# Kernel optimization log

Measured on AMD Instinct MI355X. Metric: run time of the kernel, lower is better.

The kernel has to match this reference:

```python
import jax, jax.numpy as jnp
import numpy as np

INPUT_DIM = 512
OUTPUT_DIM = 128
MAX_DEPTH = 5          # internal nodes at depths 0..4, leaves at depth 5
BATCH = 16384
N_INT = 2**MAX_DEPTH - 1        # 31 internal nodes (heap order: node i children 2i+1, 2i+2)
N_ALL = 2**(MAX_DEPTH + 1) - 1  # 63 nodes total, each owns a leaf vector


def setup_inputs() -> dict:
    key = jax.random.key(0)
    k0, k1, k2, k3, k4 = jax.random.split(key, 5)
    x = jax.random.normal(k0, (BATCH, INPUT_DIM), dtype=jnp.float32)
    lim = 1.0 / np.sqrt(INPUT_DIM)  # torch nn.Linear default init range
    W = jax.random.uniform(k1, (N_INT, 2, INPUT_DIM), jnp.float32, -lim, lim)
    b = jax.random.uniform(k2, (N_INT, 2), jnp.float32, -lim, lim)
    # gamma initialized to [0.5, 0.5] in the module; perturb slightly so it's not degenerate
    gamma = 0.5 + 0.02 * jax.random.normal(k3, (N_INT, 2), dtype=jnp.float32)
    leaf = jax.random.normal(k4, (N_ALL, OUTPUT_DIM), dtype=jnp.float32)
    return {"x": x, "W": W, "b": b, "gamma": gamma, "leaf": leaf}


def reference(x, W, b, gamma, leaf):
    """Level-by-level (bottom-up) vectorized evaluation of the recursive MixNode tree.

    Per internal node n (heap-indexed):
      router = softmax(x @ W[n].T + b[n])                      # soft routing path of route()
      children = left * router[:,0] + right * router[:,1]      # stack + bmm
      g = softmax(gamma[n])
      y = g[0] * children + g[1] * leaf[n]                     # stack + matmul(gamma)
    Pure leaves (depth == max_depth) return leaf broadcast over batch.
    """
    B = x.shape[0]
    # depth-5 pure leaves: heap indices 31..62 -> Y: [B, 32, O]
    Y = jnp.broadcast_to(leaf[N_INT:N_ALL][None], (B, 2**MAX_DEPTH, leaf.shape[-1]))
    for d in range(MAX_DEPTH - 1, -1, -1):
        s, e = 2**d - 1, 2**(d + 1) - 1   # internal nodes at depth d
        logits = jnp.einsum('bi,nji->bnj', x, W[s:e]) + b[s:e]   # [B, 2^d, 2]
        r = jax.nn.softmax(logits, axis=-1)
        left, right = Y[:, 0::2], Y[:, 1::2]                      # children in heap order
        comb = left * r[..., 0:1] + right * r[..., 1:2]           # [B, 2^d, O]
        g = jax.nn.softmax(gamma[s:e], axis=-1)                   # [2^d, 2]
        Y = g[None, :, 0:1] * comb + g[None, :, 1:2] * leaf[s:e][None]
    return Y[:, 0]  # root output [B, O]
```

## Files before the change

kernel.cpp:

```cpp
#include <hip/hip_runtime.h>
#include <hip/hip_bf16.h>
#include <cstdint>

#define BATCH   16384
#define INDIM   512
#define OUTDIM  128
#define NINT    31
#define BM      64
#define THREADS 1024

#define WS_WBF    0u
#define WS_LEAFT  65536u
#define WS_BIAS   81920u
#define WS_GSM0   82176u
#define WS_GSM1   82432u

typedef __attribute__((ext_vector_type(8))) short s8v;
typedef __attribute__((ext_vector_type(4))) float f4v;

__device__ __forceinline__ short bfs(float f) {
    return (short)__builtin_bit_cast(unsigned short, __float2bfloat16(f));
}
__device__ __forceinline__ unsigned int pk2(float lo, float hi) {
    return (unsigned int)(unsigned short)bfs(lo) |
           ((unsigned int)(unsigned short)bfs(hi) << 16);
}

#define SWZ(r, k) ((k) ^ (((r) & 7) << 3))

__global__ __launch_bounds__(256) void prep_kernel(
    const float* __restrict__ W, const float* __restrict__ bvec,
    const float* __restrict__ gamma, const float* __restrict__ leaf,
    unsigned char* __restrict__ ws)
{
    unsigned short* wbf = (unsigned short*)(ws + WS_WBF);
    unsigned short* lT  = (unsigned short*)(ws + WS_LEAFT);
    float* bias = (float*)(ws + WS_BIAS);
    float* g0v  = (float*)(ws + WS_GSM0);
    float* g1v  = (float*)(ws + WS_GSM1);
    const int tid  = blockIdx.x * 256 + threadIdx.x;
    const int nthr = gridDim.x * 256;

    for (int i = tid; i < 64 * INDIM; i += nthr) {
        int r = i >> 9;
        float v = (r < 62) ? W[i] : 0.0f;
        wbf[i] = (unsigned short)bfs(v);
    }
    for (int i = tid; i < OUTDIM * 64; i += nthr) {
        int n = i & 63, col = i >> 6;
        float v = (n < 63) ? leaf[(size_t)n * OUTDIM + col] : 0.0f;
        lT[i] = (unsigned short)bfs(v);
    }
    if (tid < 64) bias[tid] = (tid < 62) ? bvec[tid] : 0.0f;
    if (tid < NINT) {
        float a = gamma[2*tid], b = gamma[2*tid+1];
        float m = fmaxf(a, b);
        float e0 = __expf(a - m), e1 = __expf(b - m);
        float inv = 1.0f / (e0 + e1);
        g0v[tid] = e0 * inv;
        g1v[tid] = e1 * inv;
    }
}

__global__ __launch_bounds__(THREADS) void mix_main(
    const float* __restrict__ x, const unsigned char* __restrict__ ws,
    float* __restrict__ out)
{
    __shared__ __align__(16) float Lgp[4][BM][65];
    __shared__ __align__(16) unsigned short cbf[BM][64];
    __shared__ float gsh0[NINT], gsh1[NINT];

    const int t    = threadIdx.x;
    const int lane = t & 63;
    const int w    = t >> 6;
    const int rg   = w & 3;
    const int kg   = w >> 2;
    const int g    = lane >> 4;
    const int lm   = lane & 15;
    const int row0 = blockIdx.x * BM;

    if (t < NINT) {
        gsh0[t] = ((const float*)(ws + WS_GSM0))[t];
        gsh1[t] = ((const float*)(ws + WS_GSM1))[t];
    }

    const float* bias = (const float*)(ws + WS_BIAS);
    f4v acc[4];
    #pragma unroll
    for (int c = 0; c < 4; ++c) {
        float b = (kg == 0) ? bias[16*c + lm] : 0.0f;
        acc[c] = (f4v){b, b, b, b};
    }

    const float* xrow = x + (size_t)(row0 + 16*rg + lm) * INDIM + 128*kg;
    const unsigned short* wb = (const unsigned short*)(ws + WS_WBF) + 128*kg;
    #pragma unroll
    for (int ks = 0; ks < 4; ++ks) {
        const int k0 = ks * 32 + 8 * g;
        float4 x0 = *(const float4*)(xrow + k0);
        float4 x1 = *(const float4*)(xrow + k0 + 4);
        s8v a;
        a[0] = bfs(x0.x); a[1] = bfs(x0.y); a[2] = bfs(x0.z); a[3] = bfs(x0.w);
        a[4] = bfs(x1.x); a[5] = bfs(x1.y); a[6] = bfs(x1.z); a[7] = bfs(x1.w);
        #pragma unroll
        for (int c = 0; c < 4; ++c) {
            s8v b = *(const s8v*)(wb + (size_t)(16*c + lm) * INDIM + k0);
            acc[c] = __builtin_amdgcn_mfma_f32_16x16x32_bf16(a, b, acc[c], 0, 0, 0);
        }
    }
    #pragma unroll
    for (int c = 0; c < 4; ++c)
        #pragma unroll
        for (int r = 0; r < 4; ++r)
            Lgp[kg][16*rg + 4*g + r][16*c + lm] = acc[c][r];
    __syncthreads();

    {
        const int row = t >> 4;
        const int c0  = (t & 15) * 4;
        #pragma unroll
        for (int j = 0; j < 4; ++j) {
            const int c = c0 + j;
            Lgp[0][row][c] += Lgp[1][row][c] + Lgp[2][row][c] + Lgp[3][row][c];
        }
    }
    __syncthreads();

    if (t < BM) {
        const int row = t;
        float Pp[63];
        unsigned int cvp[32];
        float sv = 0.0f;
        Pp[0] = 1.0f;
        #pragma unroll
        for (int n = 0; n < NINT; ++n) {
            float l0 = Lgp[0][row][2*n];
            float l1 = Lgp[0][row][2*n + 1];
            float r1 = 1.0f / (1.0f + __expf(l0 - l1));
            float base = Pp[n] * gsh0[n];
            Pp[2*n + 1] = base * (1.0f - r1);
            Pp[2*n + 2] = base * r1;
            float cval = Pp[n] * gsh1[n];
            if (n & 1) cvp[n >> 1] = pk2(sv, cval); else sv = cval;
        }
        #pragma unroll
        for (int n = NINT; n < 63; ++n) {
            float cval = Pp[n];
            if (n & 1) cvp[n >> 1] = pk2(sv, cval); else sv = cval;
        }
        cvp[31] = pk2(sv, 0.0f);
        #pragma unroll
        for (int j = 0; j < 8; ++j) {
            int p = SWZ(row, 8 * j);
            *(uint4*)&cbf[row][p] =
                make_uint4(cvp[4*j], cvp[4*j+1], cvp[4*j+2], cvp[4*j+3]);
        }
    }
    __syncthreads();

    const unsigned short* lT = (const unsigned short*)(ws + WS_LEAFT);
    f4v o[2] = {};
    #pragma unroll
    for (int kw = 0; kw < 2; ++kw) {
        const int k0 = kw * 32 + 8 * g;
        s8v a = *(const s8v*)&cbf[16*rg + lm][SWZ(lm, k0)];
        #pragma unroll
        for (int j = 0; j < 2; ++j) {
            s8v b = *(const s8v*)(lT + (size_t)(16*(2*kg + j) + lm) * 64 + k0);
            o[j] = __builtin_amdgcn_mfma_f32_16x16x32_bf16(a, b, o[j], 0, 0, 0);
        }
    }
    #pragma unroll
    for (int j = 0; j < 2; ++j)
        #pragma unroll
        for (int r = 0; r < 4; ++r)
            out[(size_t)(row0 + 16*rg + 4*g + r) * OUTDIM + 16*(2*kg + j) + lm] = o[j][r];
}

extern "C" void kernel_launch(void* const* d_in, const int* in_sizes, int n_in,
                              void* d_out, int out_size, void* d_ws, size_t ws_size,
                              hipStream_t stream) {
    const float* x     = (const float*)d_in[0];
    const float* W     = (const float*)d_in[1];
    const float* b     = (const float*)d_in[2];
    const float* gamma = (const float*)d_in[3];
    const float* leaf  = (const float*)d_in[4];
    float* out = (float*)d_out;
    hipLaunchKernelGGL(prep_kernel, dim3(128), dim3(256), 0, stream,
                       W, b, gamma, leaf, (unsigned char*)d_ws);
    hipLaunchKernelGGL(mix_main, dim3(BATCH / BM), dim3(THREADS), 0, stream,
                       x, (const unsigned char*)d_ws, out);
}
```

Baseline: 96.03 us.

## Fuse prep kernel into main kernel and halve block size

Result: slower. 98.17 us (+2.2%).

```diff
diff --git a/kernel.cpp b/kernel.cpp
--- a/kernel.cpp
+++ b/kernel.cpp
@@ -7,13 +7,7 @@
 #define OUTDIM  128
 #define NINT    31
 #define BM      64
-#define THREADS 1024
-
-#define WS_WBF    0u
-#define WS_LEAFT  65536u
-#define WS_BIAS   81920u
-#define WS_GSM0   82176u
-#define WS_GSM1   82432u
+#define THREADS 512
 
 typedef __attribute__((ext_vector_type(8))) short s8v;
 typedef __attribute__((ext_vector_type(4))) float f4v;
@@ -28,45 +22,13 @@
 
 #define SWZ(r, k) ((k) ^ (((r) & 7) << 3))
 
-__global__ __launch_bounds__(256) void prep_kernel(
-    const float* __restrict__ W, const float* __restrict__ bvec,
-    const float* __restrict__ gamma, const float* __restrict__ leaf,
-    unsigned char* __restrict__ ws)
+__global__ __launch_bounds__(THREADS) void mix_fused(
+    const float* __restrict__ x, const float* __restrict__ W,
+    const float* __restrict__ bvec, const float* __restrict__ gamma,
+    const float* __restrict__ leaf, float* __restrict__ out)
 {
-    unsigned short* wbf = (unsigned short*)(ws + WS_WBF);
-    unsigned short* lT  = (unsigned short*)(ws + WS_LEAFT);
-    float* bias = (float*)(ws + WS_BIAS);
-    float* g0v  = (float*)(ws + WS_GSM0);
-    float* g1v  = (float*)(ws + WS_GSM1);
-    const int tid  = blockIdx.x * 256 + threadIdx.x;
-    const int nthr = gridDim.x * 256;
-
-    for (int i = tid; i < 64 * INDIM; i += nthr) {
-        int r = i >> 9;
-        float v = (r < 62) ? W[i] : 0.0f;
-        wbf[i] = (unsigned short)bfs(v);
-    }
-    for (int i = tid; i < OUTDIM * 64; i += nthr) {
-        int n = i & 63, col = i >> 6;
-        float v = (n < 63) ? leaf[(size_t)n * OUTDIM + col] : 0.0f;
-        lT[i] = (unsigned short)bfs(v);
-    }
-    if (tid < 64) bias[tid] = (tid < 62) ? bvec[tid] : 0.0f;
-    if (tid < NINT) {
-        float a = gamma[2*tid], b = gamma[2*tid+1];
-        float m = fmaxf(a, b);
-        float e0 = __expf(a - m), e1 = __expf(b - m);
-        float inv = 1.0f / (e0 + e1);
-        g0v[tid] = e0 * inv;
-        g1v[tid] = e1 * inv;
-    }
-}
-
-__global__ __launch_bounds__(THREADS) void mix_main(
-    const float* __restrict__ x, const unsigned char* __restrict__ ws,
-    float* __restrict__ out)
-{
-    __shared__ __align__(16) float Lgp[4][BM][65];
+    __shared__ __align__(16) float Lgp[2][BM][65];
+    __shared__ __align__(16) unsigned short leafT[OUTDIM][64];
     __shared__ __align__(16) unsigned short cbf[BM][64];
     __shared__ float gsh0[NINT], gsh1[NINT];
 
@@ -74,28 +36,47 @@
     const int lane = t & 63;
     const int w    = t >> 6;
     const int rg   = w & 3;
-    const int kg   = w >> 2;
+    const int kh   = w >> 2;
     const int g    = lane >> 4;
     const int lm   = lane & 15;
     const int row0 = blockIdx.x * BM;
 
+    for (int f = t; f < 63 * 32; f += THREADS) {
+        int n  = f >> 5;
+        int c4 = f & 31;
+        float4 lv = *(const float4*)(leaf + (size_t)n * OUTDIM + c4 * 4);
+        int col = c4 * 4;
+        leafT[col+0][SWZ(col+0, n)] = (unsigned short)bfs(lv.x);
+        leafT[col+1][SWZ(col+1, n)] = (unsigned short)bfs(lv.y);
+        leafT[col+2][SWZ(col+2, n)] = (unsigned short)bfs(lv.z);
+        leafT[col+3][SWZ(col+3, n)] = (unsigned short)bfs(lv.w);
+    }
+    if (t < OUTDIM) leafT[t][SWZ(t, 63)] = 0;
     if (t < NINT) {
-        gsh0[t] = ((const float*)(ws + WS_GSM0))[t];
-        gsh1[t] = ((const float*)(ws + WS_GSM1))[t];
+        float a = gamma[2*t], b = gamma[2*t+1];
+        float m = fmaxf(a, b);
+        float e0 = __expf(a - m), e1 = __expf(b - m);
+        float inv = 1.0f / (e0 + e1);
+        gsh0[t] = e0 * inv;
+        gsh1[t] = e1 * inv;
     }
 
-    const float* bias = (const float*)(ws + WS_BIAS);
     f4v acc[4];
     #pragma unroll
     for (int c = 0; c < 4; ++c) {
-        float b = (kg == 0) ? bias[16*c + lm] : 0.0f;
+        int col = 16*c + lm;
+        float b = (kh == 0 && col < 62) ? bvec[col] : 0.0f;
         acc[c] = (f4v){b, b, b, b};
     }
-
-    const float* xrow = x + (size_t)(row0 + 16*rg + lm) * INDIM + 128*kg;
-    const unsigned short* wb = (const unsigned short*)(ws + WS_WBF) + 128*kg;
+    const float* xrow = x + (size_t)(row0 + 16*rg + lm) * INDIM + 256*kh;
+    const float* wp[4];
     #pragma unroll
-    for (int ks = 0; ks < 4; ++ks) {
+    for (int c = 0; c < 4; ++c) {
+        int wr = 16*c + lm;
+        wp[c] = W + (size_t)(wr < 62 ? wr : 61) * INDIM + 256*kh;
+    }
+    #pragma unroll
+    for (int ks = 0; ks < 8; ++ks) {
         const int k0 = ks * 32 + 8 * g;
         float4 x0 = *(const float4*)(xrow + k0);
         float4 x1 = *(const float4*)(xrow + k0 + 4);
@@ -104,7 +85,11 @@
         a[4] = bfs(x1.x); a[5] = bfs(x1.y); a[6] = bfs(x1.z); a[7] = bfs(x1.w);
         #pragma unroll
         for (int c = 0; c < 4; ++c) {
-            s8v b = *(const s8v*)(wb + (size_t)(16*c + lm) * INDIM + k0);
+            float4 w0 = *(const float4*)(wp[c] + k0);
+            float4 w1 = *(const float4*)(wp[c] + k0 + 4);
+            s8v b;
+            b[0] = bfs(w0.x); b[1] = bfs(w0.y); b[2] = bfs(w0.z); b[3] = bfs(w0.w);
+            b[4] = bfs(w1.x); b[5] = bfs(w1.y); b[6] = bfs(w1.z); b[7] = bfs(w1.w);
             acc[c] = __builtin_amdgcn_mfma_f32_16x16x32_bf16(a, b, acc[c], 0, 0, 0);
         }
     }
@@ -112,17 +97,15 @@
     for (int c = 0; c < 4; ++c)
         #pragma unroll
         for (int r = 0; r < 4; ++r)
-            Lgp[kg][16*rg + 4*g + r][16*c + lm] = acc[c][r];
+            Lgp[kh][16*rg + 4*g + r][16*c + lm] = acc[c][r];
     __syncthreads();
 
     {
-        const int row = t >> 4;
-        const int c0  = (t & 15) * 4;
+        const int row = t >> 3;
+        const int c0  = (t & 7) * 8;
         #pragma unroll
-        for (int j = 0; j < 4; ++j) {
-            const int c = c0 + j;
-            Lgp[0][row][c] += Lgp[1][row][c] + Lgp[2][row][c] + Lgp[3][row][c];
-        }
+        for (int j = 0; j < 8; ++j)
+            Lgp[0][row][c0 + j] += Lgp[1][row][c0 + j];
     }
     __syncthreads();
 
@@ -158,23 +141,23 @@
     }
     __syncthreads();
 
-    const unsigned short* lT = (const unsigned short*)(ws + WS_LEAFT);
-    f4v o[2] = {};
+    f4v o[4] = {};
     #pragma unroll
     for (int kw = 0; kw < 2; ++kw) {
         const int k0 = kw * 32 + 8 * g;
         s8v a = *(const s8v*)&cbf[16*rg + lm][SWZ(lm, k0)];
         #pragma unroll
-        for (int j = 0; j < 2; ++j) {
-            s8v b = *(const s8v*)(lT + (size_t)(16*(2*kg + j) + lm) * 64 + k0);
+        for (int j = 0; j < 4; ++j) {
+            const int colr = 16*(4*kh + j) + lm;
+            s8v b = *(const s8v*)&leafT[colr][SWZ(lm, k0)];
             o[j] = __builtin_amdgcn_mfma_f32_16x16x32_bf16(a, b, o[j], 0, 0, 0);
         }
     }
     #pragma unroll
-    for (int j = 0; j < 2; ++j)
+    for (int j = 0; j < 4; ++j)
         #pragma unroll
         for (int r = 0; r < 4; ++r)
-            out[(size_t)(row0 + 16*rg + 4*g + r) * OUTDIM + 16*(2*kg + j) + lm] = o[j][r];
+            out[(size_t)(row0 + 16*rg + 4*g + r) * OUTDIM + 16*(4*kh + j) + lm] = o[j][r];
 }
 
 extern "C" void kernel_launch(void* const* d_in, const int* in_sizes, int n_in,
@@ -186,8 +169,6 @@
     const float* gamma = (const float*)d_in[3];
     const float* leaf  = (const float*)d_in[4];
     float* out = (float*)d_out;
-    hipLaunchKernelGGL(prep_kernel, dim3(128), dim3(256), 0, stream,
-                       W, b, gamma, leaf, (unsigned char*)d_ws);
-    hipLaunchKernelGGL(mix_main, dim3(BATCH / BM), dim3(THREADS), 0, stream,
-                       x, (const unsigned char*)d_ws, out);
+    hipLaunchKernelGGL(mix_fused, dim3(BATCH / BM), dim3(THREADS), 0, stream,
+                       x, W, b, gamma, leaf, out);
 }
```
